# Kernel optimization log

Measured on AMD Instinct MI355X. Metric: run time of the kernel, lower is better.

The kernel has to match this reference:

```python
import jax, jax.numpy as jnp
import numpy as np

NUM_NETS = 100_000
PINS_PER_NET = 8
NUM_PINS = NUM_NETS * PINS_PER_NET
XL, XH, YL, YH = 0.0, 512.0, 0.0, 512.0
NBX, NBY = 256, 256
BSX = (XH - XL) / NBX  # 2.0
BSY = (YH - YL) / NBY  # 2.0
UNIT_HCAP, UNIT_VCAP = 50.0, 40.0


def setup_inputs() -> dict:
    key = jax.random.key(0)
    k1, k2, k3, k4, k5 = jax.random.split(key, 5)
    # pin positions in xyxy... order, uniform inside the layout region
    pin_pos = jax.random.uniform(k1, (2 * NUM_PINS,), jnp.float32, XL, XH)
    # CSR net -> pin map: uniform degree for realism/simplicity
    netpin_start = (jnp.arange(NUM_NETS + 1, dtype=jnp.int32) * PINS_PER_NET)
    flat_netpin = jax.random.permutation(k2, jnp.arange(NUM_PINS, dtype=jnp.int32))
    net_weights = jax.random.uniform(k3, (NUM_NETS,), jnp.float32, 0.5, 1.5)
    init_h = jax.random.uniform(k4, (NBX, NBY), jnp.float32) * 0.1
    init_v = jax.random.uniform(k5, (NBX, NBY), jnp.float32) * 0.1
    return {
        "pin_pos": pin_pos,
        "netpin_start": netpin_start,
        "flat_netpin": flat_netpin,
        "net_weights": net_weights,
        "initial_horizontal_utilization_map": init_h,
        "initial_vertical_utilization_map": init_v,
    }


def _rudy_maps(pin_pos, netpin_start, flat_netpin, net_weights):
    P = flat_netpin.shape[0]
    # map each flat pin entry to its net id from the CSR offsets
    pin2net = jnp.searchsorted(netpin_start, jnp.arange(P, dtype=netpin_start.dtype), side="right") - 1
    px = pin_pos[2 * flat_netpin]
    py = pin_pos[2 * flat_netpin + 1]
    # per-net bounding boxes
    xmin = jax.ops.segment_min(px, pin2net, num_segments=NUM_NETS)
    xmax = jax.ops.segment_max(px, pin2net, num_segments=NUM_NETS)
    ymin = jax.ops.segment_min(py, pin2net, num_segments=NUM_NETS)
    ymax = jax.ops.segment_max(py, pin2net, num_segments=NUM_NETS)
    # 1D overlaps of each net bbox with each bin interval (separable)
    bin_lo_x = XL + jnp.arange(NBX, dtype=pin_pos.dtype) * BSX
    bin_lo_y = YL + jnp.arange(NBY, dtype=pin_pos.dtype) * BSY
    ox = jnp.clip(jnp.minimum(xmax[:, None], bin_lo_x[None, :] + BSX)
                  - jnp.maximum(xmin[:, None], bin_lo_x[None, :]), 0.0)  # [N, NBX]
    oy = jnp.clip(jnp.minimum(ymax[:, None], bin_lo_y[None, :] + BSY)
                  - jnp.maximum(ymin[:, None], bin_lo_y[None, :]), 0.0)  # [N, NBY]
    # RUDY: horizontal demand density = wt / bbox_height, vertical = wt / bbox_width,
    # deposited proportionally to bbox-bin overlap area.
    wt_h = net_weights / (ymax - ymin)
    wt_v = net_weights / (xmax - xmin)
    H = jnp.einsum("nx,ny->xy", ox * wt_h[:, None], oy)  # [NBX, NBY]
    V = jnp.einsum("nx,ny->xy", ox * wt_v[:, None], oy)
    return H, V


def reference(pin_pos, netpin_start, flat_netpin, net_weights,
              initial_horizontal_utilization_map, initial_vertical_utilization_map):
    H, V = _rudy_maps(pin_pos, netpin_start, flat_netpin, net_weights)
    bin_area = BSX * BSY
    H = H * (1.0 / (bin_area * UNIT_HCAP)) + initial_horizontal_utilization_map
    V = V * (1.0 / (bin_area * UNIT_VCAP)) + initial_vertical_utilization_map
    route = jnp.maximum(jnp.abs(H), jnp.abs(V))
    return route, H, V
```

## Files before the change

kernel.cpp:

```cpp
#include <hip/hip_runtime.h>
#include <hip/hip_bf16.h>


#define NBX 256
#define NBY 256
#define NMAP (NBX * NBY)
#define NPAIR 128
#define SL 8
#define CAP 12288

constexpr float BSX = 2.0f;
constexpr float BSY = 2.0f;
constexpr float INV_H = 1.0f / (4.0f * 50.0f);
constexpr float INV_V = 1.0f / (4.0f * 40.0f);

__device__ __forceinline__ float seg_cum(float t, float mn, float mx) {
    return fminf(fmaxf(t, mn), mx) - mn;
}
__device__ __forceinline__ float second_diff(int i, float bs, float mn, float mx) {
    float u2 = seg_cum((float)(i + 1) * bs, mn, mx);
    float u1 = seg_cum((float)(i) * bs, mn, mx);
    float u0 = seg_cum((float)(i - 1) * bs, mn, mx);
    return (u2 - u1) - (u1 - u0);
}
__device__ __forceinline__ int net_pairs(float4 bb, int* pl) {
    if (bb.y < bb.x) return 0;
    int i0 = (int)floorf(bb.x * 0.5f);
    int i1 = (int)floorf(bb.y * 0.5f);
    int a = i0 >> 1, b = (i0 + 1) >> 1, c = i1 >> 1, d = (i1 + 1) >> 1;
    int n = 0;
    pl[n++] = a;
    if (b != a && b < NPAIR) pl[n++] = b;
    if (c != a && c != b) pl[n++] = c;
    if (d != a && d != b && d != c && d < NPAIR) pl[n++] = d;
    return n;
}

__global__ void zero_ctrl(unsigned* __restrict__ ctrl) {
    ctrl[threadIdx.x] = 0u;
}

__global__ void __launch_bounds__(256) bbox_place(
    const float* __restrict__ pin_pos,
    const int* __restrict__ netpin_start,
    const int* __restrict__ flat_netpin,
    const float* __restrict__ net_weights,
    float4* __restrict__ rec,
    unsigned* __restrict__ gcursor,
    int* __restrict__ bucket,
    int num_nets) {
    __shared__ unsigned cnt[NPAIR], base[NPAIR], loc[NPAIR];
    const int tid = threadIdx.x;
    const int n = blockIdx.x * 256 + tid;
    if (tid < NPAIR) { cnt[tid] = 0u; loc[tid] = 0u; }
    __syncthreads();

    int pl[4];
    int k = 0;
    if (n < num_nets) {
        int s = netpin_start[n], e = netpin_start[n + 1];
        float xmn = 3.0e38f, xmx = -3.0e38f, ymn = 3.0e38f, ymx = -3.0e38f;
        if (e - s == 8 && (s & 3) == 0) {
            int4 a = *reinterpret_cast<const int4*>(flat_netpin + s);
            int4 b = *reinterpret_cast<const int4*>(flat_netpin + s + 4);
            int idx[8] = {a.x, a.y, a.z, a.w, b.x, b.y, b.z, b.w};
#pragma unroll
            for (int p = 0; p < 8; ++p) {
                float2 xy = *reinterpret_cast<const float2*>(pin_pos + 2 * (size_t)idx[p]);
                xmn = fminf(xmn, xy.x);
                xmx = fmaxf(xmx, xy.x);
                ymn = fminf(ymn, xy.y);
                ymx = fmaxf(ymx, xy.y);
            }
        } else {
            for (int p = s; p < e; ++p) {
                int ip = flat_netpin[p];
                float2 xy = *reinterpret_cast<const float2*>(pin_pos + 2 * (size_t)ip);
                xmn = fminf(xmn, xy.x);
                xmx = fmaxf(xmx, xy.x);
                ymn = fminf(ymn, xy.y);
                ymx = fmaxf(ymx, xy.y);
            }
        }
        float4 bb = (e <= s) ? make_float4(3.0e38f, -3.0e38f, 3.0e38f, -3.0e38f)
                             : make_float4(xmn, xmx, ymn, ymx);
        float w = (n < num_nets && e > s) ? net_weights[n] : 0.0f;
        rec[2 * (size_t)n]     = bb;
        rec[2 * (size_t)n + 1] = make_float4(w / (bb.w - bb.z),
                                             w / (bb.y - bb.x),
                                             0.f, 0.f);
        k = net_pairs(bb, pl);
    }
    for (int i = 0; i < k; ++i) atomicAdd(&cnt[pl[i]], 1u);
    __syncthreads();
    if (tid < NPAIR && cnt[tid])
        base[tid] = atomicAdd(&gcursor[tid], cnt[tid]);
    __syncthreads();
    for (int i = 0; i < k; ++i) {
        int p = pl[i];
        unsigned slot = base[p] + atomicAdd(&loc[p], 1u);
        if (slot < CAP) bucket[p * CAP + slot] = n;
    }
}

__global__ void __launch_bounds__(256) pair_build_sliced(
    const float4* __restrict__ rec,
    const unsigned* __restrict__ gcursor,
    const int* __restrict__ bucket,
    float2* __restrict__ Dpart) {
    __shared__ float h0[NBY], v0[NBY], h1[NBY], v1[NBY];
    const int pair  = blockIdx.x & (NPAIR - 1);
    const int slice = blockIdx.x >> 7;
    const int tid = threadIdx.x;
    h0[tid] = 0.f; v0[tid] = 0.f; h1[tid] = 0.f; v1[tid] = 0.f;
    __syncthreads();

    const int r0 = pair * 2, r1 = r0 + 1;
    const int boff = pair * CAP;
    unsigned cu = gcursor[pair];
    const int cnt = (int)(cu > CAP ? CAP : cu);
    const int span = (cnt + SL - 1) / SL;
    const int beg = slice * span;
    const int end = min(beg + span, cnt);

    auto deposit = [&](int id) {
        float4 bb = rec[2 * (size_t)id];
        float4 wt = rec[2 * (size_t)id + 1];
        float dA = second_diff(r0, BSX, bb.x, bb.y);
        float dB = second_diff(r1, BSX, bb.x, bb.y);
        int j0 = (int)floorf(bb.z * 0.5f);
        int j1 = (int)floorf(bb.w * 0.5f);
        int yi[4];
        yi[0] = j0;
        yi[1] = j0 + 1;
        yi[2] = (j1 > j0 + 1) ? j1 : -1;
        yi[3] = (j1 > j0) ? j1 + 1 : -1;
#pragma unroll
        for (int c2 = 0; c2 < 4; ++c2) {
            int y = yi[c2];
            if (y >= 0 && y < NBY) {
                float dy = second_diff(y, BSY, bb.z, bb.w);
                if (dy != 0.0f) {
                    if (dA != 0.0f) {
                        atomicAdd(&h0[y], wt.x * dA * dy);
                        atomicAdd(&v0[y], wt.y * dA * dy);
                    }
                    if (dB != 0.0f) {
                        atomicAdd(&h1[y], wt.x * dB * dy);
                        atomicAdd(&v1[y], wt.y * dB * dy);
                    }
                }
            }
        }
    };

    int q = beg + tid;
    for (; q + 768 < end; q += 1024) {
        int a = bucket[boff + q];
        int b = bucket[boff + q + 256];
        int c = bucket[boff + q + 512];
        int d = bucket[boff + q + 768];
        deposit(a);
        deposit(b);
        deposit(c);
        deposit(d);
    }
    for (; q < end; q += 256) deposit(bucket[boff + q]);
    __syncthreads();

    size_t sb = (size_t)slice * NMAP;
    Dpart[sb + (size_t)r0 * NBY + tid] = make_float2(h0[tid], v0[tid]);
    Dpart[sb + (size_t)r1 * NBY + tid] = make_float2(h1[tid], v1[tid]);
}

__global__ void __launch_bounds__(256) fold_rows_scan(
    const float2* __restrict__ Dpart,
    float2* __restrict__ D) {
    __shared__ float bh[NBY];
    __shared__ float bv[NBY];
    int r = blockIdx.x, y = threadIdx.x;
    float h = 0.f, v = 0.f;
#pragma unroll
    for (int s = 0; s < SL; ++s) {
        float2 t = Dpart[(size_t)s * NMAP + (size_t)r * NBY + y];
        h += t.x;
        v += t.y;
    }
    bh[y] = h;
    bv[y] = v;
    __syncthreads();
    for (int off = 1; off < NBY; off <<= 1) {
        float ah = (y >= off) ? bh[y - off] : 0.f;
        float av = (y >= off) ? bv[y - off] : 0.f;
        __syncthreads();
        bh[y] += ah;
        bv[y] += av;
        __syncthreads();
    }
    D[(size_t)r * NBY + y] = make_float2(bh[y], bv[y]);
}

__global__ void __launch_bounds__(256) scan_cols_finalize(
    const float2* __restrict__ D,
    const float* __restrict__ init_h,
    const float* __restrict__ init_v,
    float* __restrict__ out) {
    __shared__ float bh[NBX];
    __shared__ float bv[NBX];
    int y = blockIdx.x;
    int x = threadIdx.x;
    float2 t = D[x * NBY + y];
    bh[x] = t.x;
    bv[x] = t.y;
    __syncthreads();
    for (int off = 1; off < NBX; off <<= 1) {
        float ah = (x >= off) ? bh[x - off] : 0.f;
        float av = (x >= off) ? bv[x - off] : 0.f;
        __syncthreads();
        bh[x] += ah;
        bv[x] += av;
        __syncthreads();
    }
    int idx = x * NBY + y;
    float H = fmaf(bh[x], INV_H, init_h[idx]);
    float V = fmaf(bv[x], INV_V, init_v[idx]);
    float r = fmaxf(fabsf(H), fabsf(V));
    out[idx]            = r;
    out[idx + NMAP]     = H;
    out[idx + 2 * NMAP] = V;
}

extern "C" void kernel_launch(void* const* d_in, const int* in_sizes, int n_in,
                              void* d_out, int out_size, void* d_ws, size_t ws_size,
                              hipStream_t stream) {
    const float* pin_pos      = (const float*)d_in[0];
    const int*   netpin_start = (const int*)d_in[1];
    const int*   flat_netpin  = (const int*)d_in[2];
    const float* net_weights  = (const float*)d_in[3];
    const float* init_h       = (const float*)d_in[4];
    const float* init_v       = (const float*)d_in[5];
    float* out = (float*)d_out;

    int num_nets = in_sizes[3];
    int Np = (num_nets + 255) & ~255;

    char* w = (char*)d_ws;
    size_t o = 0;
    float4*   rec    = (float4*)(w + o);   o += (size_t)Np * 32;
    int*      bucket = (int*)(w + o);      o += (size_t)NPAIR * CAP * 4;
    float2*   Dpart  = (float2*)(w + o);   o += (size_t)SL * NMAP * 8;
    float2*   D      = (float2*)(w + o);   o += (size_t)NMAP * 8;
    unsigned* ctrl   = (unsigned*)(w + o); o += 512;

    zero_ctrl<<<1, NPAIR, 0, stream>>>(ctrl);
    bbox_place<<<Np / 256, 256, 0, stream>>>(pin_pos, netpin_start, flat_netpin,
                                             net_weights, rec, ctrl, bucket,
                                             num_nets);
    pair_build_sliced<<<NPAIR * SL, 256, 0, stream>>>(rec, ctrl, bucket, Dpart);
    fold_rows_scan<<<NBX, 256, 0, stream>>>(Dpart, D);
    scan_cols_finalize<<<NBY, 256, 0, stream>>>(D, init_h, init_v, out);
}
```

Measured before the change: 97.76 us.

## Replace y-axis difference scatter and scan with dense per-bin overlap accumulation

The pair-building kernel used to scatter second differences along y into shared memory with atomics, which then required a prefix scan over each row. Now each thread owns one y bin and accumulates the exact y overlap of every bucketed net into registers. Per-net x coefficients are staged in shared memory in tiles of 256. This removes the shared atomics and the row scan in the fold kernel, at the cost of each thread touching every net in the slice. The weight load also drops its num_nets bound check and relies on padded nets having an empty CSR range.

```diff
diff --git a/kernel.cpp b/kernel.cpp
--- a/kernel.cpp
+++ b/kernel.cpp
@@ -16,12 +16,6 @@
 
 __device__ __forceinline__ float seg_cum(float t, float mn, float mx) {
     return fminf(fmaxf(t, mn), mx) - mn;
-}
-__device__ __forceinline__ float second_diff(int i, float bs, float mn, float mx) {
-    float u2 = seg_cum((float)(i + 1) * bs, mn, mx);
-    float u1 = seg_cum((float)(i) * bs, mn, mx);
-    float u0 = seg_cum((float)(i - 1) * bs, mn, mx);
-    return (u2 - u1) - (u1 - u0);
 }
 __device__ __forceinline__ int net_pairs(float4 bb, int* pl) {
     if (bb.y < bb.x) return 0;
@@ -84,7 +78,7 @@
         }
         float4 bb = (e <= s) ? make_float4(3.0e38f, -3.0e38f, 3.0e38f, -3.0e38f)
                              : make_float4(xmn, xmx, ymn, ymx);
-        float w = (n < num_nets && e > s) ? net_weights[n] : 0.0f;
+        float w = (e > s) ? net_weights[n] : 0.0f;
         rec[2 * (size_t)n]     = bb;
         rec[2 * (size_t)n + 1] = make_float4(w / (bb.w - bb.z),
                                              w / (bb.y - bb.x),
@@ -103,17 +97,16 @@
     }
 }
 
-__global__ void __launch_bounds__(256) pair_build_sliced(
+__global__ void __launch_bounds__(256) pair_build_dense(
     const float4* __restrict__ rec,
     const unsigned* __restrict__ gcursor,
     const int* __restrict__ bucket,
     float2* __restrict__ Dpart) {
-    __shared__ float h0[NBY], v0[NBY], h1[NBY], v1[NBY];
+    __shared__ float2 sy[256];
+    __shared__ float4 sc[256];
     const int pair  = blockIdx.x & (NPAIR - 1);
     const int slice = blockIdx.x >> 7;
     const int tid = threadIdx.x;
-    h0[tid] = 0.f; v0[tid] = 0.f; h1[tid] = 0.f; v1[tid] = 0.f;
-    __syncthreads();
 
     const int r0 = pair * 2, r1 = r0 + 1;
     const int boff = pair * CAP;
@@ -123,61 +116,49 @@
     const int beg = slice * span;
     const int end = min(beg + span, cnt);
 
-    auto deposit = [&](int id) {
-        float4 bb = rec[2 * (size_t)id];
-        float4 wt = rec[2 * (size_t)id + 1];
-        float dA = second_diff(r0, BSX, bb.x, bb.y);
-        float dB = second_diff(r1, BSX, bb.x, bb.y);
-        int j0 = (int)floorf(bb.z * 0.5f);
-        int j1 = (int)floorf(bb.w * 0.5f);
-        int yi[4];
-        yi[0] = j0;
-        yi[1] = j0 + 1;
-        yi[2] = (j1 > j0 + 1) ? j1 : -1;
-        yi[3] = (j1 > j0) ? j1 + 1 : -1;
-#pragma unroll
-        for (int c2 = 0; c2 < 4; ++c2) {
-            int y = yi[c2];
-            if (y >= 0 && y < NBY) {
-                float dy = second_diff(y, BSY, bb.z, bb.w);
-                if (dy != 0.0f) {
-                    if (dA != 0.0f) {
-                        atomicAdd(&h0[y], wt.x * dA * dy);
-                        atomicAdd(&v0[y], wt.y * dA * dy);
-                    }
-                    if (dB != 0.0f) {
-                        atomicAdd(&h1[y], wt.x * dB * dy);
-                        atomicAdd(&v1[y], wt.y * dB * dy);
-                    }
-                }
-            }
+    float h0 = 0.f, v0 = 0.f, h1 = 0.f, v1 = 0.f;
+    const float lo = (float)tid * BSY;
+    const float hi = lo + BSY;
+
+    for (int t0 = beg; t0 < end; t0 += 256) {
+        const int m = min(256, end - t0);
+        if (tid < m) {
+            int id = bucket[boff + t0 + tid];
+            float4 bb = rec[2 * (size_t)id];
+            float4 wt = rec[2 * (size_t)id + 1];
+            float e0 = seg_cum((float)(r0 - 1) * BSX, bb.x, bb.y);
+            float e1 = seg_cum((float)(r0)     * BSX, bb.x, bb.y);
+            float e2 = seg_cum((float)(r1)     * BSX, bb.x, bb.y);
+            float e3 = seg_cum((float)(r1 + 1) * BSX, bb.x, bb.y);
+            float dA = (e2 - e1) - (e1 - e0);
+            float dB = (e3 - e2) - (e2 - e1);
+            sy[tid] = make_float2(bb.z, bb.w);
+            sc[tid] = make_float4(dA != 0.f ? wt.x * dA : 0.f,
+                                  dA != 0.f ? wt.y * dA : 0.f,
+                                  dB != 0.f ? wt.x * dB : 0.f,
+                                  dB != 0.f ? wt.y * dB : 0.f);
         }
-    };
-
-    int q = beg + tid;
-    for (; q + 768 < end; q += 1024) {
-        int a = bucket[boff + q];
-        int b = bucket[boff + q + 256];
-        int c = bucket[boff + q + 512];
-        int d = bucket[boff + q + 768];
-        deposit(a);
-        deposit(b);
-        deposit(c);
-        deposit(d);
-    }
-    for (; q < end; q += 256) deposit(bucket[boff + q]);
-    __syncthreads();
-
+        __syncthreads();
+#pragma unroll 4
+        for (int j = 0; j < m; ++j) {
+            float2 yy = sy[j];
+            float4 c  = sc[j];
+            float oy = fmaxf(0.f, fminf(yy.y, hi) - fmaxf(yy.x, lo));
+            h0 = fmaf(c.x, oy, h0);
+            v0 = fmaf(c.y, oy, v0);
+            h1 = fmaf(c.z, oy, h1);
+            v1 = fmaf(c.w, oy, v1);
+        }
+        __syncthreads();
+    }
     size_t sb = (size_t)slice * NMAP;
-    Dpart[sb + (size_t)r0 * NBY + tid] = make_float2(h0[tid], v0[tid]);
-    Dpart[sb + (size_t)r1 * NBY + tid] = make_float2(h1[tid], v1[tid]);
-}
-
-__global__ void __launch_bounds__(256) fold_rows_scan(
+    Dpart[sb + (size_t)r0 * NBY + tid] = make_float2(h0, v0);
+    Dpart[sb + (size_t)r1 * NBY + tid] = make_float2(h1, v1);
+}
+
+__global__ void __launch_bounds__(256) fold_rows(
     const float2* __restrict__ Dpart,
     float2* __restrict__ D) {
-    __shared__ float bh[NBY];
-    __shared__ float bv[NBY];
     int r = blockIdx.x, y = threadIdx.x;
     float h = 0.f, v = 0.f;
 #pragma unroll
@@ -186,18 +167,7 @@
         h += t.x;
         v += t.y;
     }
-    bh[y] = h;
-    bv[y] = v;
-    __syncthreads();
-    for (int off = 1; off < NBY; off <<= 1) {
-        float ah = (y >= off) ? bh[y - off] : 0.f;
-        float av = (y >= off) ? bv[y - off] : 0.f;
-        __syncthreads();
-        bh[y] += ah;
-        bv[y] += av;
-        __syncthreads();
-    }
-    D[(size_t)r * NBY + y] = make_float2(bh[y], bv[y]);
+    D[(size_t)r * NBY + y] = make_float2(h, v);
 }
 
 __global__ void __launch_bounds__(256) scan_cols_finalize(
@@ -256,7 +226,7 @@
     bbox_place<<<Np / 256, 256, 0, stream>>>(pin_pos, netpin_start, flat_netpin,
                                              net_weights, rec, ctrl, bucket,
                                              num_nets);
-    pair_build_sliced<<<NPAIR * SL, 256, 0, stream>>>(rec, ctrl, bucket, Dpart);
-    fold_rows_scan<<<NBX, 256, 0, stream>>>(Dpart, D);
+    pair_build_dense<<<NPAIR * SL, 256, 0, stream>>>(rec, ctrl, bucket, Dpart);
+    fold_rows<<<NBX, 256, 0, stream>>>(Dpart, D);
     scan_cols_finalize<<<NBY, 256, 0, stream>>>(D, init_h, init_v, out);
 }
```

Result: slower. 110.6 us (+13.1%).
